# Optimization experiments

Measured on AMD Instinct MI355X. Metric: run time of the kernel, lower is better.

## Reference

```python
import jax, jax.numpy as jnp
import numpy as np

B, T, F, H = 1024, 100, 64, 256


def _unif(key, shape, stdv):
    return jax.random.uniform(key, shape, jnp.float32, -stdv, stdv)


def setup_inputs() -> dict:
    key = jax.random.key(0)
    ks = jax.random.split(key, 20)
    X = jax.random.normal(ks[0], (B, T, F), jnp.float32)
    missing_mask = jnp.round(jax.random.uniform(ks[1], (B, T, F), jnp.float32))
    deltas = jax.random.uniform(ks[2], (B, T, F), jnp.float32)
    s_h = 1.0 / np.sqrt(H)
    s_f = 1.0 / np.sqrt(F)
    return {
        "X": X, "missing_mask": missing_mask, "deltas": deltas,
        # TemporalDecay h: W [H,F], b [H] (stdv = 1/sqrt(out=H))
        "W_dh": _unif(ks[3], (H, F), s_h), "b_dh": _unif(ks[4], (H,), s_h),
        # TemporalDecay x (diag): W [F,F], b [F]
        "W_dx": _unif(ks[5], (F, F), s_f), "b_dx": _unif(ks[6], (F,), s_f),
        # hist_reg: Linear(H -> F)
        "W_hist": _unif(ks[7], (F, H), s_h), "b_hist": _unif(ks[8], (F,), s_h),
        # feat_reg: W [F,F] masked by (1 - I), b [F]
        "W_feat": _unif(ks[9], (F, F), s_f), "b_feat": _unif(ks[10], (F,), s_f),
        # weight_combine: Linear(2F -> F)
        "W_comb": _unif(ks[11], (F, 2 * F), 1.0 / np.sqrt(2 * F)),
        "b_comb": _unif(ks[12], (F,), 1.0 / np.sqrt(2 * F)),
        # LSTMCell(2F -> H): gates order i,f,g,o
        "W_ih": _unif(ks[13], (4 * H, 2 * F), s_h), "b_ih": _unif(ks[14], (4 * H,), s_h),
        "W_hh": _unif(ks[15], (4 * H, H), s_h), "b_hh": _unif(ks[16], (4 * H,), s_h),
    }


def _masked_mae(inp, tgt, mask):
    return jnp.sum(jnp.abs(inp - tgt) * mask) / (jnp.sum(mask) + 1e-9)


def _rits(X, missing_mask, deltas, W_dh, b_dh, W_dx, b_dx, W_hist, b_hist,
          W_feat, b_feat, W_comb, b_comb, W_ih, b_ih, W_hh, b_hh):
    f = X.shape[-1]
    w_dx_diag = jnp.diag(W_dx)                       # diag TemporalDecay: W * eye
    W_feat_m = W_feat * (1.0 - jnp.eye(f, dtype=W_feat.dtype))

    def step(carry, xt):
        h, c, rec_loss, rec_mae = carry
        x, m, d = xt                                  # each [B, F]
        gamma_h = jnp.exp(-jax.nn.relu(d @ W_dh.T + b_dh))   # [B, H]
        gamma_x = jnp.exp(-jax.nn.relu(d * w_dx_diag + b_dx))  # [B, F]
        h = h * gamma_h
        x_h = h @ W_hist.T + b_hist
        rec_loss = rec_loss + _masked_mae(x_h, x, m)
        x_c = m * x + (1.0 - m) * x_h
        z_h = x_c @ W_feat_m.T + b_feat
        rec_loss = rec_loss + _masked_mae(z_h, x, m)
        alpha = jax.nn.sigmoid(jnp.concatenate([gamma_x, m], axis=1) @ W_comb.T + b_comb)
        c_h = alpha * z_h + (1.0 - alpha) * x_h
        rec_mae = rec_mae + _masked_mae(c_h, x, m)
        rec_loss = rec_loss + rec_mae                 # faithful to source (cumulative MAE added)
        c_c = m * x + (1.0 - m) * c_h
        inputs = jnp.concatenate([c_c, m], axis=1)    # [B, 2F]
        gates = inputs @ W_ih.T + b_ih + h @ W_hh.T + b_hh
        i_g, f_g, g_g, o_g = jnp.split(gates, 4, axis=1)
        c = jax.nn.sigmoid(f_g) * c + jax.nn.sigmoid(i_g) * jnp.tanh(g_g)
        h = jax.nn.sigmoid(o_g) * jnp.tanh(c)
        return (h, c, rec_loss, rec_mae), c_h

    b = X.shape[0]
    hsz = W_hh.shape[1]
    init = (jnp.zeros((b, hsz), X.dtype), jnp.zeros((b, hsz), X.dtype),
            jnp.asarray(0.0, X.dtype), jnp.asarray(0.0, X.dtype))
    xs = (jnp.swapaxes(X, 0, 1), jnp.swapaxes(missing_mask, 0, 1), jnp.swapaxes(deltas, 0, 1))
    (h, c, rec_loss, rec_mae), ests = jax.lax.scan(step, init, xs)
    estimations = jnp.swapaxes(ests, 0, 1)            # [B, T, F]
    imputed = missing_mask * X + (1.0 - missing_mask) * estimations
    seq_len = X.shape[1]
    return imputed, rec_mae / seq_len, rec_loss / (seq_len * 3)


def reference(X, missing_mask, deltas, W_dh, b_dh, W_dx, b_dx, W_hist, b_hist,
              W_feat, b_feat, W_comb, b_comb, W_ih, b_ih, W_hh, b_hh):
    return _rits(X, missing_mask, deltas, W_dh, b_dh, W_dx, b_dx, W_hist, b_hist,
                 W_feat, b_feat, W_comb, b_comb, W_ih, b_ih, W_hh, b_hh)
```

## Files before the change

kernel.cpp:

```cpp
#include <hip/hip_runtime.h>
#include <hip/hip_bf16.h>


#define Bz 1024
#define Tz 100
#define Fz 64
#define Hz 256
#define GROUPS 64
#define SIBS 4
#define RPB 16

typedef __attribute__((ext_vector_type(8))) short short8;
typedef __attribute__((ext_vector_type(4))) float floatx4;
typedef __hip_bfloat16 bf16;
typedef unsigned long long u64;

#define MFMA16(a, b, c) __builtin_amdgcn_mfma_f32_16x16x32_bf16((a), (b), (c), 0, 0, 0)

__device__ __forceinline__ float sigmf(float x) { return 1.0f / (1.0f + __expf(-x)); }
__device__ __forceinline__ float tanhfast(float x) { return 2.0f / (1.0f + __expf(-2.0f * x)) - 1.0f; }


__global__ void rits_convert(const float* __restrict__ Wdh, const float* __restrict__ Wdx,
                             const float* __restrict__ Whist, const float* __restrict__ Wfeat,
                             const float* __restrict__ Wcomb, const float* __restrict__ Wih,
                             const float* __restrict__ Whh, bf16* __restrict__ wsbf,
                             float* __restrict__ wdxd, unsigned int* __restrict__ flagsArr) {
    int idx = blockIdx.x * blockDim.x + threadIdx.x;
    if (idx < 4096) flagsArr[idx] = 0u;
    if (idx < 64) wdxd[idx] = Wdx[idx * 65];
    if (idx >= 438272) return;
    float v;
    if (idx < 16384) v = Wdh[idx];
    else if (idx < 32768) v = Whist[idx - 16384];
    else if (idx < 36864) { int i = idx - 32768; v = ((i >> 6) == (i & 63)) ? 0.0f : Wfeat[i]; }
    else if (idx < 45056) v = Wcomb[idx - 36864];
    else {
        int i = idx - 45056;
        int e = i & 7, q = (i >> 3) & 3, l = (i >> 5) & 15, g = (i >> 9) & 3, w = (i >> 11) & 15;
        int s = i >> 15;
        int n = g * 256 + w * 16 + l;
        v = (s < 4) ? Wih[n * 128 + s * 32 + q * 8 + e] : Whh[n * 256 + (s - 4) * 32 + q * 8 + e];
    }
    wsbf[idx] = __float2bfloat16(v);
}

__global__ __launch_bounds__(1024, 4) void rits_main(
    const float* __restrict__ X, const float* __restrict__ Mm, const float* __restrict__ Dd,
    const float* __restrict__ b_dh, const float* __restrict__ b_dx,
    const float* __restrict__ b_hist, const float* __restrict__ b_feat,
    const float* __restrict__ b_comb, const float* __restrict__ b_ih,
    const float* __restrict__ b_hh,
    const bf16* __restrict__ Wdh, const bf16* __restrict__ Whist,
    const bf16* __restrict__ Wfeatm, const bf16* __restrict__ Wcomb,
    const bf16* __restrict__ Wp5,
    const float* __restrict__ wdxd, float* __restrict__ lossbuf,
    unsigned int* __restrict__ flags, u64* __restrict__ pub, float* __restrict__ out) {
    __shared__ __align__(16) bf16 lw_hist[64 * 264];
    __shared__ __align__(16) bf16 lw_comb[64 * 136];
    __shared__ __align__(16) bf16 lw_feat[64 * 72];
    __shared__ __align__(16) bf16 lw_dh[64 * 72];
    __shared__ __align__(16) bf16 sh_hbf[RPB * 264];
    __shared__ __align__(16) float sh_x[RPB * 64];
    __shared__ __align__(16) float sh_m[RPB * 64];
    __shared__ __align__(16) bf16 sh_dbf2[RPB * 72];
    __shared__ __align__(16) bf16 sh_xcbf[RPB * 72];
    __shared__ __align__(16) bf16 sh_gmbf[RPB * 136];
    __shared__ __align__(16) bf16 sh_inbf[RPB * 136];
    __shared__ __align__(16) float sh_alpha[RPB * 68];
    __shared__ __align__(16) float sh_gam[RPB * 68];
    __shared__ __align__(16) float sh_g[4 * 16 * 66];
    __shared__ __align__(16) float sh_c[64 * 16];
    __shared__ float sh_lred[16];
    __shared__ float sh_msum[16];

    const int tid = threadIdx.x;
    const int lane = tid & 63;
    const int wid = tid >> 6;
    const int l16 = lane & 15;
    const int q = lane >> 4;
    const int j = blockIdx.x & 3;
    const int grp = blockIdx.x >> 2;
    const int b0 = grp * RPB;

    for (int i = tid; i < 64 * 256; i += 1024) lw_hist[(i >> 8) * 264 + (i & 255)] = Whist[i];
    for (int i = tid; i < 64 * 128; i += 1024) lw_comb[(i >> 7) * 136 + (i & 127)] = Wcomb[i];
    for (int i = tid; i < 64 * 64; i += 1024) {
        lw_feat[(i >> 6) * 72 + (i & 63)] = Wfeatm[i];
        lw_dh[(i >> 6) * 72 + (i & 63)] = Wdh[(j * 64 + (i >> 6)) * 64 + (i & 63)];
    }
    for (int i = tid; i < 64 * 16; i += 1024) sh_c[i] = 0.0f;
    for (int i = tid; i < RPB * 264; i += 1024) sh_hbf[i] = (bf16)0.0f;

    const int gate = wid >> 2;
    const int ct = wid & 3;
    const int nrow = gate * 256 + j * 64 + ct * 16 + l16;
    short8 wfrag[12];
#pragma unroll
    for (int s = 0; s < 12; ++s)
        wfrag[s] = *(const short8*)(Wp5 + (size_t)s * 32768 + (j * 4 + ct) * 2048 + gate * 512 +
                                    l16 * 32 + q * 8);
    const float bgate = b_ih[nrow] + b_hh[nrow];

    const float wdxf = wdxd[lane];
    const float bdxf = b_dx[lane];
    const int ca = wid * 16 + l16;
    const int colF = (wid - 4) * 16 + l16;
    const int colg = (wid - 8) * 16 + l16;
    float bc2 = 0.f, bhl = 0.f, bft = 0.f, bdl = 0.f;
    if (wid < 4) bc2 = b_comb[ca];
    else if (wid < 8) { bhl = b_hist[colF]; bft = b_feat[colF]; }
    else if (wid < 12) bdl = b_dh[j * 64 + colg];

    const size_t g0 = (size_t)(b0 + wid) * Tz * Fz + lane;
    float xv = X[g0], mv = Mm[g0], dv = Dd[g0];

    __syncthreads();

    {
        u64* pub0 = pub + (size_t)grp * 2 * 1024;
        if (tid < 256) {
            int col = tid >> 2, qq = tid & 3;
            __hip_atomic_store(pub0 + (size_t)(j * 64 + col) * 4 + qq, 0ull, __ATOMIC_RELAXED,
                               __HIP_MEMORY_SCOPE_AGENT);
        }
        asm volatile("s_waitcnt vmcnt(0)" ::: "memory");
        if (tid < 256 && lane == 0)
            __hip_atomic_store(&flags[((grp * 4 + j) * 4 + wid) * 4], 1u, __ATOMIC_RELAXED,
                               __HIP_MEMORY_SCOPE_AGENT);
    }

    for (int t = 0; t < Tz; ++t) {
        const bool lossStep = ((t & 3) == j);
        u64* pubt = pub + ((size_t)grp * 2 + (t & 1)) * 1024;

        {
            const int row = wid, f = lane;
            sh_x[row * 64 + f] = xv;
            sh_m[row * 64 + f] = mv;
            float gx = __expf(-fmaxf(dv * wdxf + bdxf, 0.0f));
            sh_gmbf[row * 136 + f] = __float2bfloat16(gx);
            bf16 mb = __float2bfloat16(mv);
            sh_gmbf[row * 136 + 64 + f] = mb;
            sh_inbf[row * 136 + 64 + f] = mb;
            if (lossStep) {
                float v0 = mv;
#pragma unroll
                for (int off = 32; off; off >>= 1) v0 += __shfl_xor(v0, off, 64);
                if (lane == 0) sh_msum[wid] = v0;
            }
        }
        if (t + 1 < Tz) {
            size_t g = g0 + (size_t)(t + 1) * Fz;
            xv = X[g]; mv = Mm[g]; dv = Dd[g];
        }
        if (tid < 12) {
            int sidx = tid >> 2;
            int sib = sidx + (sidx >= j);
            int w = tid & 3;
            const unsigned target = (unsigned)(t + 1);
            unsigned it = 0;
            while (__hip_atomic_load(&flags[((grp * 4 + sib) * 4 + w) * 4], __ATOMIC_RELAXED,
                                     __HIP_MEMORY_SCOPE_AGENT) < target) {
                __builtin_amdgcn_s_sleep(1);
                if (++it > (1u << 22)) break;
            }
        }
        __syncthreads();

        if (tid < 768) {
            int sidx = tid >> 8;
            int sib = sidx + (sidx >= j);
            int c = sib * 64 + ((tid >> 2) & 63);
            int qq = tid & 3;
            u64 v = __hip_atomic_load(pubt + (size_t)c * 4 + qq, __ATOMIC_RELAXED,
                                      __HIP_MEMORY_SCOPE_AGENT);
            unsigned short* hb = (unsigned short*)sh_hbf;
#pragma unroll
            for (int r = 0; r < 4; ++r) hb[(qq * 4 + r) * 264 + c] = (unsigned short)(v >> (16 * r));
        }
        __syncthreads();

        floatx4 acc5 = {0.f, 0.f, 0.f, 0.f};
        float xh[4];
        float l1 = 0.f, l2 = 0.f, l3 = 0.f;
        if (wid >= 4 && wid < 8) {
            floatx4 acc = {0.f, 0.f, 0.f, 0.f};
#pragma unroll
            for (int kb = 0; kb < 8; ++kb) {
                short8 a = *(const short8*)(sh_hbf + l16 * 264 + kb * 32 + q * 8);
                short8 b = *(const short8*)(lw_hist + colF * 264 + kb * 32 + q * 8);
                acc = MFMA16(a, b, acc);
            }
#pragma unroll
            for (int r = 0; r < 4; ++r) {
                int row = q * 4 + r;
                xh[r] = acc[r] + bhl;
                float xx = sh_x[row * 64 + colF], mm = sh_m[row * 64 + colF];
                l1 += fabsf(xh[r] - xx) * mm;
                float xc = mm * xx + (1.0f - mm) * xh[r];
                sh_xcbf[row * 72 + colF] = __float2bfloat16(xc);
            }
        } else {
            if (wid < 4) {
                floatx4 acca = {0.f, 0.f, 0.f, 0.f};
#pragma unroll
                for (int kb = 0; kb < 4; ++kb) {
                    short8 a = *(const short8*)(sh_gmbf + l16 * 136 + kb * 32 + q * 8);
                    short8 b = *(const short8*)(lw_comb + ca * 136 + kb * 32 + q * 8);
                    acca = MFMA16(a, b, acca);
                }
#pragma unroll
                for (int r = 0; r < 4; ++r) sh_alpha[(q * 4 + r) * 68 + ca] = sigmf(acca[r] + bc2);
            }
#pragma unroll
            for (int s = 2; s < 4; ++s) {
                short8 a = *(const short8*)(sh_inbf + l16 * 136 + s * 32 + q * 8);
                acc5 = MFMA16(a, wfrag[s], acc5);
            }
#pragma unroll
            for (int s = 4; s < 12; ++s) {
                short8 a = *(const short8*)(sh_hbf + l16 * 264 + (s - 4) * 32 + q * 8);
                acc5 = MFMA16(a, wfrag[s], acc5);
            }
        }
        if (t + 1 < Tz) sh_dbf2[wid * 72 + lane] = __float2bfloat16(dv);
        __syncthreads();

        if (wid >= 4 && wid < 8) {
            floatx4 accz = {0.f, 0.f, 0.f, 0.f};
            {
                short8 a = *(const short8*)(sh_xcbf + l16 * 72 + q * 8);
                accz = MFMA16(a, *(const short8*)(lw_feat + colF * 72 + q * 8), accz);
                a = *(const short8*)(sh_xcbf + l16 * 72 + 32 + q * 8);
                accz = MFMA16(a, *(const short8*)(lw_feat + colF * 72 + 32 + q * 8), accz);
            }
#pragma unroll
            for (int r = 0; r < 4; ++r) {
                int row = q * 4 + r;
                float xx = sh_x[row * 64 + colF], mm = sh_m[row * 64 + colF];
                float z = accz[r] + bft;
                l2 += fabsf(z - xx) * mm;
                float al = sh_alpha[row * 68 + colF];
                float ch = al * z + (1.0f - al) * xh[r];
                l3 += fabsf(ch - xx) * mm;
                float imp = mm * xx + (1.0f - mm) * ch;
                if (wid - 4 == j) out[((size_t)(b0 + row) * Tz + t) * Fz + colF] = imp;
                sh_inbf[row * 136 + colF] = __float2bfloat16(imp);
            }
            if (lossStep) {
                float v1 = l1, v2 = l2, v3 = l3;
#pragma unroll
                for (int off = 32; off; off >>= 1) {
                    v1 += __shfl_xor(v1, off, 64);
                    v2 += __shfl_xor(v2, off, 64);
                    v3 += __shfl_xor(v3, off, 64);
                }
                if (lane == 0) {
                    sh_lred[(wid - 4) * 4 + 0] = v1;
                    sh_lred[(wid - 4) * 4 + 1] = v2;
                    sh_lred[(wid - 4) * 4 + 2] = v3;
                }
            }
        } else if (wid >= 8 && wid < 12 && t + 1 < Tz) {
            short8 a0 = *(const short8*)(sh_dbf2 + l16 * 72 + q * 8);
            short8 a1 = *(const short8*)(sh_dbf2 + l16 * 72 + 32 + q * 8);
            short8 w0 = *(const short8*)(lw_dh + colg * 72 + q * 8);
            short8 w1 = *(const short8*)(lw_dh + colg * 72 + 32 + q * 8);
            floatx4 acc = {0.f, 0.f, 0.f, 0.f};
            acc = MFMA16(a0, w0, acc);
            acc = MFMA16(a1, w1, acc);
#pragma unroll
            for (int r = 0; r < 4; ++r)
                sh_gam[(q * 4 + r) * 68 + colg] = __expf(-fmaxf(acc[r] + bdl, 0.0f));
        }
        __syncthreads();

        {
#pragma unroll
            for (int s = 0; s < 2; ++s) {
                short8 a = *(const short8*)(sh_inbf + l16 * 136 + s * 32 + q * 8);
                acc5 = MFMA16(a, wfrag[s], acc5);
            }
#pragma unroll
            for (int r = 0; r < 4; ++r) {
                float v = acc5[r] + bgate;
                float tv = (gate == 2) ? tanhfast(v) : sigmf(v);
                sh_g[(gate * 16 + q * 4 + r) * 66 + ct * 16 + l16] = tv;
            }
        }
        __syncthreads();

        if (tid < 256) {
            int col = tid >> 2, q2 = tid & 3;
            int gcol = j * 64 + col;
            float4 cv = *(float4*)(sh_c + col * 16 + q2 * 4);
            float cc[4] = {cv.x, cv.y, cv.z, cv.w};
            u64 pk = 0;
#pragma unroll
            for (int r = 0; r < 4; ++r) {
                int row = q2 * 4 + r;
                float Ig = sh_g[(0 * 16 + row) * 66 + col];
                float Fg = sh_g[(1 * 16 + row) * 66 + col];
                float Gg = sh_g[(2 * 16 + row) * 66 + col];
                float Og = sh_g[(3 * 16 + row) * 66 + col];
                float c = Fg * cc[r] + Ig * Gg;
                cc[r] = c;
                if (t + 1 < Tz) {
                    float h = Og * tanhfast(c);
                    float hd = h * sh_gam[row * 68 + col];
                    bf16 hb = __float2bfloat16(hd);
                    sh_hbf[row * 264 + gcol] = hb;
                    pk |= (u64)(*(unsigned short*)&hb) << (16 * r);
                }
            }
            *(float4*)(sh_c + col * 16 + q2 * 4) = (float4){cc[0], cc[1], cc[2], cc[3]};
            if (t + 1 < Tz) {
                u64* pubn = pub + ((size_t)grp * 2 + ((t + 1) & 1)) * 1024;
                __hip_atomic_store(pubn + (size_t)gcol * 4 + q2, pk, __ATOMIC_RELAXED,
                                   __HIP_MEMORY_SCOPE_AGENT);
            }
        }
        if (tid < 256 && t + 1 < Tz) {
            asm volatile("s_waitcnt vmcnt(0)" ::: "memory");
            if (lane == 0)
                __hip_atomic_store(&flags[((grp * 4 + j) * 4 + wid) * 4], (unsigned)(t + 2),
                                   __ATOMIC_RELAXED, __HIP_MEMORY_SCOPE_AGENT);
        }
        if (tid == 256 && lossStep) {
            float s0 = 0.0f;
#pragma unroll
            for (int i = 0; i < 16; ++i) s0 += sh_msum[i];
            float* lb = lossbuf + ((size_t)grp * Tz + t) * 4;
            lb[0] = s0;
            lb[1] = sh_lred[0] + sh_lred[4] + sh_lred[8] + sh_lred[12];
            lb[2] = sh_lred[1] + sh_lred[5] + sh_lred[9] + sh_lred[13];
            lb[3] = sh_lred[2] + sh_lred[6] + sh_lred[10] + sh_lred[14];
        }
        __syncthreads();
    }
}

__global__ void rits_finalize(const float* __restrict__ lossbuf, float* __restrict__ out) {
    __shared__ float m1[Tz], m2[Tz], m3[Tz];
    int t = threadIdx.x;
    if (t < Tz) {
        float s0 = 0.0f, s1 = 0.0f, s2 = 0.0f, s3 = 0.0f;
        for (int g = 0; g < GROUPS; ++g) {
            const float* lb = lossbuf + ((size_t)g * Tz + t) * 4;
            s0 += lb[0]; s1 += lb[1]; s2 += lb[2]; s3 += lb[3];
        }
        float inv = 1.0f / (s0 + 1e-9f);
        m1[t] = s1 * inv; m2[t] = s2 * inv; m3[t] = s3 * inv;
    }
    __syncthreads();
    if (t == 0) {
        float rm = 0.0f, rl = 0.0f;
        for (int i = 0; i < Tz; ++i) {
            rl += m1[i]; rl += m2[i]; rm += m3[i]; rl += rm;
        }
        out[(size_t)Bz * Tz * Fz] = rm / (float)Tz;
        out[(size_t)Bz * Tz * Fz + 1] = rl / (3.0f * (float)Tz);
    }
}

extern "C" void kernel_launch(void* const* d_in, const int* in_sizes, int n_in,
                              void* d_out, int out_size, void* d_ws, size_t ws_size,
                              hipStream_t stream) {
    const float* X = (const float*)d_in[0];
    const float* Mm = (const float*)d_in[1];
    const float* Dd = (const float*)d_in[2];
    const float* Wdh = (const float*)d_in[3];
    const float* b_dh = (const float*)d_in[4];
    const float* Wdx = (const float*)d_in[5];
    const float* b_dx = (const float*)d_in[6];
    const float* Whist = (const float*)d_in[7];
    const float* b_hist = (const float*)d_in[8];
    const float* Wfeat = (const float*)d_in[9];
    const float* b_feat = (const float*)d_in[10];
    const float* Wcomb = (const float*)d_in[11];
    const float* b_comb = (const float*)d_in[12];
    const float* Wih = (const float*)d_in[13];
    const float* b_ih = (const float*)d_in[14];
    const float* Whh = (const float*)d_in[15];
    const float* b_hh = (const float*)d_in[16];
    float* out = (float*)d_out;

    bf16* wsbf = (bf16*)d_ws;
    float* wdxd = (float*)((char*)d_ws + 876544);
    float* lossbuf = (float*)((char*)d_ws + 876800);
    unsigned int* flags = (unsigned int*)((char*)d_ws + 979200);
    u64* pub = (u64*)((char*)d_ws + 995584);

    rits_convert<<<1712, 256, 0, stream>>>(Wdh, Wdx, Whist, Wfeat, Wcomb, Wih, Whh, wsbf, wdxd,
                                           flags);
    rits_main<<<GROUPS * SIBS, 1024, 0, stream>>>(
        X, Mm, Dd, b_dh, b_dx, b_hist, b_feat, b_comb, b_ih, b_hh, wsbf + 0, wsbf + 16384,
        wsbf + 32768, wsbf + 36864, wsbf + 45056, wdxd, lossbuf, flags, pub, out);
    rits_finalize<<<1, 128, 0, stream>>>(lossbuf, out);
}
```

Measured before the change: 845.4 us.

## Move sibling flag wait to end of step and drop initial zero-publish barrier

The spin-wait on sibling blocks' published hidden state moves from the start of each timestep to the end of the previous one, run by an idle warp while the others finish. The cross-block load of sibling h slices is issued early in the next step, before the x/mask staging. This removes one __syncthreads and the t=0 zero-publish handshake. The goal is to shorten the per-step critical path of the inter-block exchange, at the risk of a subtle ordering change, since loads are now issued before any barrier on the current step.

Result: slower. 930.0 us (+10.0%).

```diff
diff --git a/kernel.cpp b/kernel.cpp
--- a/kernel.cpp
+++ b/kernel.cpp
@@ -117,23 +117,21 @@
 
     __syncthreads();
 
-    {
-        u64* pub0 = pub + (size_t)grp * 2 * 1024;
-        if (tid < 256) {
-            int col = tid >> 2, qq = tid & 3;
-            __hip_atomic_store(pub0 + (size_t)(j * 64 + col) * 4 + qq, 0ull, __ATOMIC_RELAXED,
-                               __HIP_MEMORY_SCOPE_AGENT);
-        }
-        asm volatile("s_waitcnt vmcnt(0)" ::: "memory");
-        if (tid < 256 && lane == 0)
-            __hip_atomic_store(&flags[((grp * 4 + j) * 4 + wid) * 4], 1u, __ATOMIC_RELAXED,
-                               __HIP_MEMORY_SCOPE_AGENT);
-    }
-
     for (int t = 0; t < Tz; ++t) {
         const bool lossStep = ((t & 3) == j);
-        u64* pubt = pub + ((size_t)grp * 2 + (t & 1)) * 1024;
-
+
+        u64 vh = 0;
+        int rc = 0, rqq = 0;
+        if (t > 0 && tid >= 256) {
+            int idx = tid - 256;
+            int sidx = idx >> 8;
+            int sib = sidx + (sidx >= j);
+            rc = sib * 64 + ((idx >> 2) & 63);
+            rqq = idx & 3;
+            const u64* pubt = pub + ((size_t)grp * 2 + (t & 1)) * 1024;
+            vh = __hip_atomic_load(pubt + (size_t)rc * 4 + rqq, __ATOMIC_RELAXED,
+                                   __HIP_MEMORY_SCOPE_AGENT);
+        }
         {
             const int row = wid, f = lane;
             sh_x[row * 64 + f] = xv;
@@ -154,30 +152,11 @@
             size_t g = g0 + (size_t)(t + 1) * Fz;
             xv = X[g]; mv = Mm[g]; dv = Dd[g];
         }
-        if (tid < 12) {
-            int sidx = tid >> 2;
-            int sib = sidx + (sidx >= j);
-            int w = tid & 3;
-            const unsigned target = (unsigned)(t + 1);
-            unsigned it = 0;
-            while (__hip_atomic_load(&flags[((grp * 4 + sib) * 4 + w) * 4], __ATOMIC_RELAXED,
-                                     __HIP_MEMORY_SCOPE_AGENT) < target) {
-                __builtin_amdgcn_s_sleep(1);
-                if (++it > (1u << 22)) break;
-            }
-        }
-        __syncthreads();
-
-        if (tid < 768) {
-            int sidx = tid >> 8;
-            int sib = sidx + (sidx >= j);
-            int c = sib * 64 + ((tid >> 2) & 63);
-            int qq = tid & 3;
-            u64 v = __hip_atomic_load(pubt + (size_t)c * 4 + qq, __ATOMIC_RELAXED,
-                                      __HIP_MEMORY_SCOPE_AGENT);
+        if (t > 0 && tid >= 256) {
             unsigned short* hb = (unsigned short*)sh_hbf;
 #pragma unroll
-            for (int r = 0; r < 4; ++r) hb[(qq * 4 + r) * 264 + c] = (unsigned short)(v >> (16 * r));
+            for (int r = 0; r < 4; ++r)
+                hb[(rqq * 4 + r) * 264 + rc] = (unsigned short)(vh >> (16 * r));
         }
         __syncthreads();
 
@@ -319,13 +298,22 @@
                 u64* pubn = pub + ((size_t)grp * 2 + ((t + 1) & 1)) * 1024;
                 __hip_atomic_store(pubn + (size_t)gcol * 4 + q2, pk, __ATOMIC_RELAXED,
                                    __HIP_MEMORY_SCOPE_AGENT);
-            }
-        }
-        if (tid < 256 && t + 1 < Tz) {
-            asm volatile("s_waitcnt vmcnt(0)" ::: "memory");
-            if (lane == 0)
-                __hip_atomic_store(&flags[((grp * 4 + j) * 4 + wid) * 4], (unsigned)(t + 2),
-                                   __ATOMIC_RELAXED, __HIP_MEMORY_SCOPE_AGENT);
+                asm volatile("s_waitcnt vmcnt(0)" ::: "memory");
+                if (lane == 0)
+                    __hip_atomic_store(&flags[((grp * 4 + j) * 4 + wid) * 4], (unsigned)(t + 2),
+                                       __ATOMIC_RELAXED, __HIP_MEMORY_SCOPE_AGENT);
+            }
+        } else if (tid >= 960 && tid < 972 && t + 1 < Tz) {
+            int sidx = (tid - 960) >> 2;
+            int sib = sidx + (sidx >= j);
+            int w = tid & 3;
+            const unsigned target = (unsigned)(t + 2);
+            unsigned it = 0;
+            while (__hip_atomic_load(&flags[((grp * 4 + sib) * 4 + w) * 4], __ATOMIC_RELAXED,
+                                     __HIP_MEMORY_SCOPE_AGENT) < target) {
+                __builtin_amdgcn_s_sleep(1);
+                if (++it > (1u << 22)) break;
+            }
         }
         if (tid == 256 && lossStep) {
             float s0 = 0.0f;
```
